# Kernel optimization log

Hardware: AMD Instinct MI355X
Metric: run time of the kernel (lower is better)

## Reference

```python
import jax, jax.numpy as jnp
import numpy as np

B, N, D = 64, 512, 128  # graphs per batch, max nodes per graph, hidden_dim


def setup_inputs() -> dict:
    key = jax.random.key(0)
    ks = jax.random.split(key, 9)
    h1 = jax.random.normal(ks[0], (B, N, D), jnp.float32)
    h2 = jax.random.normal(ks[1], (B, N, D), jnp.float32)
    s = 1.0 / np.sqrt(D)
    Wk = jax.random.normal(ks[2], (D, D), jnp.float32) * s
    bk = jax.random.normal(ks[3], (D,), jnp.float32) * s
    Wq = jax.random.normal(ks[4], (D, D), jnp.float32) * s
    bq = jax.random.normal(ks[5], (D,), jnp.float32) * s
    t = jnp.asarray(np.sqrt(1.0 / D), jnp.float32)  # self.t = sqrt(1/hidden_dim)
    len1 = jax.random.randint(ks[6], (B,), 1, N + 1, jnp.int32)
    len2 = jax.random.randint(ks[7], (B,), 1, N + 1, jnp.int32)
    return {"h1": h1, "h2": h2, "Wk": Wk, "bk": bk, "Wq": Wq, "bq": bq,
            "t": t, "len1": len1, "len2": len2}


def reference(h1, h2, Wk, bk, Wq, bq, t, len1, len2):
    # valid-node masks for the ragged (padded) graphs
    pos = jnp.arange(N)
    m1 = pos[None, :] < len1[:, None]  # [B, N]
    m2 = pos[None, :] < len2[:, None]  # [B, N]

    # k = Linear(h), q = Linear(h)  (torch Linear: x @ W.T + b)
    k1 = jnp.einsum('bnd,ed->bne', h1, Wk) + bk
    k2 = jnp.einsum('bnd,ed->bne', h2, Wk) + bk
    q1 = jnp.einsum('bnd,ed->bne', h1, Wq) + bq
    q2 = jnp.einsum('bnd,ed->bne', h2, Wq) + bq

    NEG = jnp.asarray(-1e9, h1.dtype)

    # g1 nodes attend over g2 nodes; note values == keys (k2)
    s1 = jnp.einsum('bnd,bmd->bnm', q1, k2) * t           # [B, N1, N2]
    s1 = jnp.where(m2[:, None, :], s1, NEG)
    a1 = jax.nn.softmax(s1, axis=-1)
    o1 = jnp.einsum('bnm,bmd->bnd', a1, k2) * m1[:, :, None]

    # g2 nodes attend over g1 nodes; values == k1
    s2 = jnp.einsum('bnd,bmd->bnm', q2, k1) * t           # [B, N2, N1]
    s2 = jnp.where(m1[:, None, :], s2, NEG)
    a2 = jax.nn.softmax(s2, axis=-1)
    o2 = jnp.einsum('bnm,bmd->bnd', a2, k1) * m2[:, :, None]

    return o1, o2
```

## Files before the change

kernel.cpp:

```cpp
#include <hip/hip_runtime.h>

typedef __attribute__((ext_vector_type(8))) short bf16x8;
typedef __attribute__((ext_vector_type(4))) short s16x4;
typedef __attribute__((ext_vector_type(4))) float f32x4;
typedef __attribute__((ext_vector_type(4))) int   i32x4;

#define MFMA16 __builtin_amdgcn_mfma_f32_16x16x32_bf16

#define B_ 64
#define N_ 512
#define D_ 128
#define NCHK 16
#define BUFB 16384

__device__ __forceinline__ unsigned short f2bf(float f) {
  unsigned u = __builtin_bit_cast(unsigned, f);
  u += 0x7fffu + ((u >> 16) & 1u);
  return (unsigned short)(u >> 16);
}
__device__ __forceinline__ int packbf2(float lo, float hi) {
  return (int)((unsigned)f2bf(lo) | ((unsigned)f2bf(hi) << 16));
}

__device__ __forceinline__ void gload_lds16(const void* g, void* l) {
  __builtin_amdgcn_global_load_lds((const __attribute__((address_space(1))) unsigned*)g,
                                   (__attribute__((address_space(3))) unsigned*)l, 16, 0, 0);
}

__global__ void prep_w(const float* __restrict__ Wk, const float* __restrict__ Wq,
                       short* __restrict__ wkb, short* __restrict__ wqb) {
  int i = blockIdx.x * 256 + threadIdx.x;
  if (i < D_ * D_) { wkb[i] = (short)f2bf(Wk[i]); wqb[i] = (short)f2bf(Wq[i]); }
}

__global__ __launch_bounds__(256, 2) void proj_kernel(
    const float* __restrict__ h1, const float* __restrict__ h2,
    const short* __restrict__ wkb, const short* __restrict__ wqb,
    const float* __restrict__ bk, const float* __restrict__ bq,
    short* __restrict__ k1, short* __restrict__ k2,
    short* __restrict__ q1, short* __restrict__ q2,
    short* __restrict__ k1T, short* __restrict__ k2T) {
  const int wave = threadIdx.x >> 6, lane = threadIdx.x & 63;
  const int c = lane & 15, g = lane >> 4;
  const int rw = blockIdx.x * 128 + wave * 32;
  const int inp = rw >> 15;
  const int loc = rw & 32767;
  const int b = loc >> 9, n0 = loc & 511;
  const float* __restrict__ h = inp ? h2 : h1;
  short* __restrict__ kout = inp ? k2 : k1;
  short* __restrict__ qout = inp ? q2 : q1;
  short* __restrict__ kT   = inp ? k2T : k1T;

  bf16x8 xf[2][4];
#pragma unroll
  for (int mt = 0; mt < 2; ++mt) {
    const float* hr = h + (long)(loc + mt * 16 + c) * D_;
#pragma unroll
    for (int kk = 0; kk < 4; ++kk) {
      f32x4 lo = *(const f32x4*)(hr + kk * 32 + g * 8);
      f32x4 hi = *(const f32x4*)(hr + kk * 32 + g * 8 + 4);
      bf16x8 v;
      v[0] = (short)f2bf(lo[0]); v[1] = (short)f2bf(lo[1]);
      v[2] = (short)f2bf(lo[2]); v[3] = (short)f2bf(lo[3]);
      v[4] = (short)f2bf(hi[0]); v[5] = (short)f2bf(hi[1]);
      v[6] = (short)f2bf(hi[2]); v[7] = (short)f2bf(hi[3]);
      xf[mt][kk] = v;
    }
  }

#pragma unroll
  for (int et = 0; et < 8; ++et) {
    bf16x8 wkf[4], wqf[4];
    const short* wkr = wkb + (et * 16 + c) * D_;
    const short* wqr = wqb + (et * 16 + c) * D_;
#pragma unroll
    for (int kk = 0; kk < 4; ++kk) {
      wkf[kk] = *(const bf16x8*)(wkr + kk * 32 + g * 8);
      wqf[kk] = *(const bf16x8*)(wqr + kk * 32 + g * 8);
    }
    f32x4 ak[2], aq[2], at[2];
#pragma unroll
    for (int mt = 0; mt < 2; ++mt) {
      ak[mt] = (f32x4){0.f, 0.f, 0.f, 0.f};
      aq[mt] = (f32x4){0.f, 0.f, 0.f, 0.f};
      at[mt] = (f32x4){0.f, 0.f, 0.f, 0.f};
    }
#pragma unroll
    for (int kk = 0; kk < 4; ++kk) {
#pragma unroll
      for (int mt = 0; mt < 2; ++mt) {
        ak[mt] = MFMA16(wkf[kk], xf[mt][kk], ak[mt], 0, 0, 0);
        aq[mt] = MFMA16(wqf[kk], xf[mt][kk], aq[mt], 0, 0, 0);
        at[mt] = MFMA16(xf[mt][kk], wkf[kk], at[mt], 0, 0, 0);
      }
    }
    f32x4 bkv = *(const f32x4*)(bk + et * 16 + g * 4);
    f32x4 bqv = *(const f32x4*)(bq + et * 16 + g * 4);
    float bks = bk[et * 16 + c];
#pragma unroll
    for (int mt = 0; mt < 2; ++mt) {
      s16x4 pk, pq, pt;
#pragma unroll
      for (int j = 0; j < 4; ++j) {
        pk[j] = (short)f2bf(ak[mt][j] + bkv[j]);
        pq[j] = (short)f2bf(aq[mt][j] + bqv[j]);
        pt[j] = (short)f2bf(at[mt][j] + bks);
      }
      long row = (long)(loc + mt * 16 + c);
      *(s16x4*)(kout + row * D_ + et * 16 + g * 4) = pk;
      *(s16x4*)(qout + row * D_ + et * 16 + g * 4) = pq;
      *(s16x4*)(kT + ((long)(b * D_ + et * 16 + c)) * N_ + n0 + mt * 16 + g * 4) = pt;
    }
  }
}

__global__ __launch_bounds__(128, 2) void attn_kernel(
    const short* __restrict__ k1, const short* __restrict__ k2,
    const short* __restrict__ q1, const short* __restrict__ q2,
    const short* __restrict__ k1T, const short* __restrict__ k2T,
    const float* __restrict__ tptr,
    const int* __restrict__ len1, const int* __restrict__ len2,
    float* __restrict__ out) {
  __shared__ char smem[2 * BUFB];
  const int tid = threadIdx.x;
  const int wave = tid >> 6, lane = tid & 63;
  const int c = lane & 15, g = lane >> 4;
  const int wgid = blockIdx.x;
  const int qt = wgid >> 7;
  const int bd = wgid & 127;
  const int dir = bd >> 6, b = bd & 63;
  const short* __restrict__ qp = dir ? q2 : q1;
  const short* __restrict__ kp = dir ? k1 : k2;
  const short* __restrict__ vT = dir ? k1T : k2T;
  const int lk = dir ? len1[b] : len2[b];
  const int lq = dir ? len2[b] : len1[b];
  float* __restrict__ o = out + (long)dir * B_ * N_ * D_;
  const float ts = *tptr;
  const int q0 = qt * 64 + wave * 32;

  const char* kbase = (const char*)(kp + (long)b * N_ * D_);
  const char* vbase = (const char*)(vT + (long)b * D_ * N_);

  auto stage = [&](int i) {
    char* buf = smem + BUFB * (i & 1);
#pragma unroll
    for (int j = 0; j < 4; ++j) {
      int L = j * 2048 + tid * 16;
      int row = L >> 8, off = L & 255;
      const char* gp = kbase + (i * 32 + row) * 256 + (off ^ ((row & 7) << 4));
      gload_lds16(gp, buf + j * 2048 + (wave << 10));
    }
#pragma unroll
    for (int j = 0; j < 4; ++j) {
      int L = j * 2048 + tid * 16;
      int row = L >> 6, off = L & 63;
      const char* gp = vbase + row * 1024 + i * 64 + (off ^ (((row >> 1) & 3) << 4));
      gload_lds16(gp, buf + 8192 + j * 2048 + (wave << 10));
    }
  };

  bf16x8 qf[2][4];
#pragma unroll
  for (int t = 0; t < 2; ++t) {
    const short* qrow = qp + ((long)(b * N_ + q0 + t * 16 + c)) * D_;
#pragma unroll
    for (int kk = 0; kk < 4; ++kk) qf[t][kk] = *(const bf16x8*)(qrow + kk * 32 + g * 8);
  }

  f32x4 oacc[2][8];
#pragma unroll
  for (int t = 0; t < 2; ++t)
#pragma unroll
    for (int dt = 0; dt < 8; ++dt) oacc[t][dt] = (f32x4){0.f, 0.f, 0.f, 0.f};
  float m[2] = {-3e38f, -3e38f};
  float l[2] = {0.f, 0.f};

  const int srcA = c + ((g & 1) << 5);
  const int srcB = srcA + 16;
  const bool lowhalf = (g < 2);

  stage(0);

#pragma unroll 2
  for (int ch = 0; ch < NCHK; ++ch) {
    asm volatile("s_waitcnt vmcnt(0)" ::: "memory");
    __builtin_amdgcn_sched_barrier(0);
    __builtin_amdgcn_s_barrier();
    __builtin_amdgcn_sched_barrier(0);
    if (ch + 1 < NCHK) stage(ch + 1);
    const char* buf = smem + BUFB * (ch & 1);

    f32x4 sv[2][2];
    __builtin_amdgcn_s_setprio(1);
#pragma unroll
    for (int tl = 0; tl < 2; ++tl) {
      int r = tl * 16 + c;
      const char* base = buf + (r << 8);
      int sw = (r & 7) << 4;
      f32x4 a0 = (f32x4){0.f, 0.f, 0.f, 0.f};
      f32x4 a1 = (f32x4){0.f, 0.f, 0.f, 0.f};
#pragma unroll
      for (int kk = 0; kk < 4; ++kk) {
        bf16x8 kf = *(const bf16x8*)(base + ((kk * 64 + g * 16) ^ sw));
        a0 = MFMA16(kf, qf[0][kk], a0, 0, 0, 0);
        a1 = MFMA16(kf, qf[1][kk], a1, 0, 0, 0);
      }
      sv[0][tl] = a0; sv[1][tl] = a1;
    }
    __builtin_amdgcn_s_setprio(0);

    bf16x8 pf[2];
#pragma unroll
    for (int t = 0; t < 2; ++t) {
      float pmax = -3e38f;
#pragma unroll
      for (int tl = 0; tl < 2; ++tl) {
        const int node = ch * 32 + tl * 16 + g * 4;
#pragma unroll
        for (int j = 0; j < 4; ++j) {
          float v = sv[t][tl][j] * ts;
          v = (node + j < lk) ? v : -1e9f;
          sv[t][tl][j] = v;
          pmax = fmaxf(pmax, v);
        }
      }
      pmax = fmaxf(pmax, __shfl_xor(pmax, 16));
      pmax = fmaxf(pmax, __shfl_xor(pmax, 32));
      if (!__all(pmax - m[t] <= 8.0f)) {
        float newm = fmaxf(m[t], pmax);
        float sc = __expf(m[t] - newm);
        m[t] = newm;
        l[t] *= sc;
#pragma unroll
        for (int dt = 0; dt < 8; ++dt)
#pragma unroll
          for (int j = 0; j < 4; ++j) oacc[t][dt][j] *= sc;
      }
      float sum = 0.f;
#pragma unroll
      for (int tl = 0; tl < 2; ++tl)
#pragma unroll
        for (int j = 0; j < 4; ++j) {
          float p = __expf(sv[t][tl][j] - m[t]);
          sv[t][tl][j] = p;
          sum += p;
        }
      sum += __shfl_xor(sum, 16);
      sum += __shfl_xor(sum, 32);
      l[t] += sum;

      int a0 = packbf2(sv[t][0][0], sv[t][0][1]);
      int a1 = packbf2(sv[t][0][2], sv[t][0][3]);
      int b0 = packbf2(sv[t][1][0], sv[t][1][1]);
      int b1 = packbf2(sv[t][1][2], sv[t][1][3]);
      int xa0 = __shfl(a0, srcA), xb0 = __shfl(b0, srcA);
      int xa1 = __shfl(a1, srcA), xb1 = __shfl(b1, srcA);
      int ya0 = __shfl(a0, srcB), yb0 = __shfl(b0, srcB);
      int ya1 = __shfl(a1, srcB), yb1 = __shfl(b1, srcB);
      i32x4 ui;
      ui[0] = lowhalf ? xa0 : xb0;
      ui[1] = lowhalf ? xa1 : xb1;
      ui[2] = lowhalf ? ya0 : yb0;
      ui[3] = lowhalf ? ya1 : yb1;
      pf[t] = __builtin_bit_cast(bf16x8, ui);
    }

    __builtin_amdgcn_s_setprio(1);
#pragma unroll
    for (int dt = 0; dt < 8; ++dt) {
      int row = dt * 16 + c;
      const char* vb = buf + 8192 + row * 64;
      bf16x8 vt = *(const bf16x8*)(vb + ((g * 16) ^ (((row >> 1) & 3) << 4)));
      oacc[0][dt] = MFMA16(vt, pf[0], oacc[0][dt], 0, 0, 0);
      oacc[1][dt] = MFMA16(vt, pf[1], oacc[1][dt], 0, 0, 0);
    }
    __builtin_amdgcn_s_setprio(0);
  }

#pragma unroll
  for (int t = 0; t < 2; ++t) {
    const int qg = q0 + t * 16 + c;
    const bool valid = qg < lq;
    const float rinv = 1.0f / l[t];
    float* orow = o + ((long)(b * N_ + qg)) * D_;
#pragma unroll
    for (int dt = 0; dt < 8; ++dt) {
      f32x4 vo;
#pragma unroll
      for (int j = 0; j < 4; ++j) vo[j] = valid ? oacc[t][dt][j] * rinv : 0.0f;
      *(f32x4*)(orow + dt * 16 + g * 4) = vo;
    }
  }
}

extern "C" void kernel_launch(void* const* d_in, const int* in_sizes, int n_in,
                              void* d_out, int out_size, void* d_ws, size_t ws_size,
                              hipStream_t stream) {
  const float* h1 = (const float*)d_in[0];
  const float* h2 = (const float*)d_in[1];
  const float* Wk = (const float*)d_in[2];
  const float* bk = (const float*)d_in[3];
  const float* Wq = (const float*)d_in[4];
  const float* bq = (const float*)d_in[5];
  const float* t  = (const float*)d_in[6];
  const int* len1 = (const int*)d_in[7];
  const int* len2 = (const int*)d_in[8];

  char* ws = (char*)d_ws;
  const size_t SZ = (size_t)B_ * N_ * D_ * 2;
  short* k1  = (short*)(ws + 0 * SZ);
  short* k2  = (short*)(ws + 1 * SZ);
  short* q1  = (short*)(ws + 2 * SZ);
  short* q2  = (short*)(ws + 3 * SZ);
  short* k1T = (short*)(ws + 4 * SZ);
  short* k2T = (short*)(ws + 5 * SZ);
  short* wkb = (short*)(ws + 6 * SZ);
  short* wqb = (short*)(ws + 6 * SZ + D_ * D_ * 2);

  prep_w<<<64, 256, 0, stream>>>(Wk, Wq, wkb, wqb);
  proj_kernel<<<512, 256, 0, stream>>>(h1, h2, wkb, wqb, bk, bq,
                                       k1, k2, q1, q2, k1T, k2T);
  attn_kernel<<<1024, 128, 0, stream>>>(k1, k2, q1, q2, k1T, k2T,
                                        t, len1, len2, (float*)d_out);
}
```

Before: 76.56 us.

## Skip padded key chunks and query tiles, fold scale into Wq, triple-buffer

```diff
diff --git a/kernel.cpp b/kernel.cpp
--- a/kernel.cpp
+++ b/kernel.cpp
@@ -10,7 +10,6 @@
 #define B_ 64
 #define N_ 512
 #define D_ 128
-#define NCHK 16
 #define BUFB 16384
 
 __device__ __forceinline__ unsigned short f2bf(float f) {
@@ -28,15 +27,19 @@
 }
 
 __global__ void prep_w(const float* __restrict__ Wk, const float* __restrict__ Wq,
-                       short* __restrict__ wkb, short* __restrict__ wqb) {
+                       const float* __restrict__ bq, const float* __restrict__ tptr,
+                       short* __restrict__ wkb, short* __restrict__ wqb,
+                       float* __restrict__ bqs) {
+  const float sc = tptr[0] * 1.4426950408889634f;
   int i = blockIdx.x * 256 + threadIdx.x;
-  if (i < D_ * D_) { wkb[i] = (short)f2bf(Wk[i]); wqb[i] = (short)f2bf(Wq[i]); }
+  if (i < D_ * D_) { wkb[i] = (short)f2bf(Wk[i]); wqb[i] = (short)f2bf(Wq[i] * sc); }
+  if (i < D_) bqs[i] = bq[i] * sc;
 }
 
 __global__ __launch_bounds__(256, 2) void proj_kernel(
     const float* __restrict__ h1, const float* __restrict__ h2,
     const short* __restrict__ wkb, const short* __restrict__ wqb,
-    const float* __restrict__ bk, const float* __restrict__ bq,
+    const float* __restrict__ bk, const float* __restrict__ bqs,
     short* __restrict__ k1, short* __restrict__ k2,
     short* __restrict__ q1, short* __restrict__ q2,
     short* __restrict__ k1T, short* __restrict__ k2T) {
@@ -95,7 +98,7 @@
       }
     }
     f32x4 bkv = *(const f32x4*)(bk + et * 16 + g * 4);
-    f32x4 bqv = *(const f32x4*)(bq + et * 16 + g * 4);
+    f32x4 bqv = *(const f32x4*)(bqs + et * 16 + g * 4);
     float bks = bk[et * 16 + c];
 #pragma unroll
     for (int mt = 0; mt < 2; ++mt) {
@@ -118,10 +121,9 @@
     const short* __restrict__ k1, const short* __restrict__ k2,
     const short* __restrict__ q1, const short* __restrict__ q2,
     const short* __restrict__ k1T, const short* __restrict__ k2T,
-    const float* __restrict__ tptr,
     const int* __restrict__ len1, const int* __restrict__ len2,
     float* __restrict__ out) {
-  __shared__ char smem[2 * BUFB];
+  __shared__ char smem[3 * BUFB];
   const int tid = threadIdx.x;
   const int wave = tid >> 6, lane = tid & 63;
   const int c = lane & 15, g = lane >> 4;
@@ -135,14 +137,20 @@
   const int lk = dir ? len1[b] : len2[b];
   const int lq = dir ? len2[b] : len1[b];
   float* __restrict__ o = out + (long)dir * B_ * N_ * D_;
-  const float ts = *tptr;
+
+  if (qt * 64 >= lq) {
+    f32x4 z = (f32x4){0.f, 0.f, 0.f, 0.f};
+    f32x4* op = (f32x4*)(o + ((long)(b * N_ + qt * 64)) * D_);
+#pragma unroll
+    for (int i = 0; i < 16; ++i) op[i * 128 + tid] = z;
+    return;
+  }
+
   const int q0 = qt * 64 + wave * 32;
-
   const char* kbase = (const char*)(kp + (long)b * N_ * D_);
   const char* vbase = (const char*)(vT + (long)b * D_ * N_);
 
-  auto stage = [&](int i) {
-    char* buf = smem + BUFB * (i & 1);
+  auto stage = [&](int i, char* buf) {
 #pragma unroll
     for (int j = 0; j < 4; ++j) {
       int L = j * 2048 + tid * 16;
@@ -179,16 +187,22 @@
   const int srcB = srcA + 16;
   const bool lowhalf = (g < 2);
 
-  stage(0);
-
-#pragma unroll 2
-  for (int ch = 0; ch < NCHK; ++ch) {
-    asm volatile("s_waitcnt vmcnt(0)" ::: "memory");
+  const int nch = (lk + 31) >> 5;
+  stage(0, smem);
+  if (nch > 1) stage(1, smem + BUFB);
+  int bi = 0;
+
+  for (int ch = 0; ch < nch; ++ch) {
+    if (ch + 1 < nch) { asm volatile("s_waitcnt vmcnt(8)" ::: "memory"); }
+    else              { asm volatile("s_waitcnt vmcnt(0)" ::: "memory"); }
     __builtin_amdgcn_sched_barrier(0);
     __builtin_amdgcn_s_barrier();
     __builtin_amdgcn_sched_barrier(0);
-    if (ch + 1 < NCHK) stage(ch + 1);
-    const char* buf = smem + BUFB * (ch & 1);
+    int si = bi + 2; if (si >= 3) si -= 3;
+    if (ch + 2 < nch) stage(ch + 2, smem + BUFB * si);
+    const char* buf = smem + BUFB * bi;
+    bi = (bi + 1 == 3) ? 0 : bi + 1;
+    const bool lastch = (ch == nch - 1);
 
     f32x4 sv[2][2];
     __builtin_amdgcn_s_setprio(1);
@@ -213,22 +227,28 @@
 #pragma unroll
     for (int t = 0; t < 2; ++t) {
       float pmax = -3e38f;
-#pragma unroll
-      for (int tl = 0; tl < 2; ++tl) {
-        const int node = ch * 32 + tl * 16 + g * 4;
-#pragma unroll
-        for (int j = 0; j < 4; ++j) {
-          float v = sv[t][tl][j] * ts;
-          v = (node + j < lk) ? v : -1e9f;
-          sv[t][tl][j] = v;
-          pmax = fmaxf(pmax, v);
+      if (lastch) {
+#pragma unroll
+        for (int tl = 0; tl < 2; ++tl) {
+          const int node = ch * 32 + tl * 16 + g * 4;
+#pragma unroll
+          for (int j = 0; j < 4; ++j) {
+            float v = (node + j < lk) ? sv[t][tl][j] : -1e9f;
+            sv[t][tl][j] = v;
+            pmax = fmaxf(pmax, v);
+          }
         }
+      } else {
+#pragma unroll
+        for (int tl = 0; tl < 2; ++tl)
+#pragma unroll
+          for (int j = 0; j < 4; ++j) pmax = fmaxf(pmax, sv[t][tl][j]);
       }
       pmax = fmaxf(pmax, __shfl_xor(pmax, 16));
       pmax = fmaxf(pmax, __shfl_xor(pmax, 32));
-      if (!__all(pmax - m[t] <= 8.0f)) {
+      if (!__all(pmax - m[t] <= 11.5f)) {
         float newm = fmaxf(m[t], pmax);
-        float sc = __expf(m[t] - newm);
+        float sc = exp2f(m[t] - newm);
         m[t] = newm;
         l[t] *= sc;
 #pragma unroll
@@ -241,7 +261,7 @@
       for (int tl = 0; tl < 2; ++tl)
 #pragma unroll
         for (int j = 0; j < 4; ++j) {
-          float p = __expf(sv[t][tl][j] - m[t]);
+          float p = exp2f(sv[t][tl][j] - m[t]);
           sv[t][tl][j] = p;
           sum += p;
         }
@@ -316,10 +336,11 @@
   short* k2T = (short*)(ws + 5 * SZ);
   short* wkb = (short*)(ws + 6 * SZ);
   short* wqb = (short*)(ws + 6 * SZ + D_ * D_ * 2);
-
-  prep_w<<<64, 256, 0, stream>>>(Wk, Wq, wkb, wqb);
-  proj_kernel<<<512, 256, 0, stream>>>(h1, h2, wkb, wqb, bk, bq,
+  float* bqs = (float*)(ws + 6 * SZ + 2 * D_ * D_ * 2);
+
+  prep_w<<<64, 256, 0, stream>>>(Wk, Wq, bq, t, wkb, wqb, bqs);
+  proj_kernel<<<512, 256, 0, stream>>>(h1, h2, wkb, wqb, bk, bqs,
                                        k1, k2, q1, q2, k1T, k2T);
   attn_kernel<<<1024, 128, 0, stream>>>(k1, k2, q1, q2, k1T, k2T,
-                                        t, len1, len2, (float*)d_out);
-}
+                                        len1, len2, (float*)d_out);
+}
```

Measured after the change: 94.41 us. +23.3%, slower.
